# Kernel tuning notes

Hardware: AMD Instinct MI355X
Metric: run time of the kernel (lower is better)

Reference implementation:

```python
import jax, jax.numpy as jnp
import numpy as np

NUM_HEADS = 12
DIM = 768
HEAD_DIM = DIM // NUM_HEADS
SCALE = HEAD_DIM ** -0.5
LORA_ALPHA = 1.0


def setup_inputs() -> dict:
    key = jax.random.key(0)
    ks = jax.random.split(key, 9)
    B, H, W = 1, 64, 64
    return {
        "x": jax.random.normal(ks[0], (B, H, W, DIM), jnp.float32),
        "w_qkv": jax.random.normal(ks[1], (3 * DIM, DIM), jnp.float32) * 0.02,
        "b_qkv": jax.random.normal(ks[2], (3 * DIM,), jnp.float32) * 0.02,
        "lora_A": jax.random.normal(ks[3], (12, DIM), jnp.float32) * 0.02,
        "lora_B": jax.random.normal(ks[4], (3 * DIM, 12), jnp.float32) * 0.02,
        "w_proj": jax.random.normal(ks[5], (DIM, DIM), jnp.float32) * 0.02,
        "b_proj": jax.random.normal(ks[6], (DIM,), jnp.float32) * 0.02,
        "rel_pos_h": jax.random.normal(ks[7], (2 * H - 1, HEAD_DIM), jnp.float32) * 0.02,
        "rel_pos_w": jax.random.normal(ks[8], (2 * W - 1, HEAD_DIM), jnp.float32) * 0.02,
    }


def _get_rel_pos(size: int, rel_pos: jnp.ndarray) -> jnp.ndarray:
    # q_size == k_size and rel_pos.shape[0] == 2*size-1, so no interpolation.
    coords = jnp.arange(size)[:, None] - jnp.arange(size)[None, :] + (size - 1)
    return rel_pos[coords]  # [size, size, head_dim]


def reference(x, w_qkv, b_qkv, lora_A, lora_B, w_proj, b_proj, rel_pos_h, rel_pos_w):
    B, H, W, _ = x.shape
    N = H * W
    # LoRA qkv projection: W_eff path = base + alpha * x @ (B A)^T
    qkv = x @ w_qkv.T + b_qkv + LORA_ALPHA * ((x @ lora_A.T) @ lora_B.T)
    qkv = qkv.reshape(B, N, 3, NUM_HEADS, HEAD_DIM)
    qkv = jnp.transpose(qkv, (2, 0, 3, 1, 4)).reshape(3, B * NUM_HEADS, N, HEAD_DIM)
    q, k, v = qkv[0], qkv[1], qkv[2]
    attn = jnp.einsum('bqc,bkc->bqk', q * SCALE, k)  # [B*nh, N, N]
    # decomposed relative position bias
    Rh = _get_rel_pos(H, rel_pos_h)  # [H, H, hd]
    Rw = _get_rel_pos(W, rel_pos_w)  # [W, W, hd]
    r_q = q.reshape(B * NUM_HEADS, H, W, HEAD_DIM)
    rel_h = jnp.einsum('bhwc,hkc->bhwk', r_q, Rh)
    rel_w = jnp.einsum('bhwc,wkc->bhwk', r_q, Rw)
    attn = (attn.reshape(-1, H, W, H, W)
            + rel_h[:, :, :, :, None]
            + rel_w[:, :, :, None, :]).reshape(-1, N, N)
    attn = jax.nn.softmax(attn, axis=-1)
    out = jnp.einsum('bqk,bkc->bqc', attn, v)  # [B*nh, N, hd]
    out = out.reshape(B, NUM_HEADS, H, W, HEAD_DIM)
    out = jnp.transpose(out, (0, 2, 3, 1, 4)).reshape(B, H, W, DIM)
    return out @ w_proj.T + b_proj
```

## Files before the change

### kernel.cpp

```cpp
#include <hip/hip_runtime.h>
#include <stdint.h>


typedef __attribute__((ext_vector_type(4))) float f32x4;
typedef __attribute__((ext_vector_type(16))) float f32x16;
typedef __attribute__((ext_vector_type(4))) float fvec4;
typedef __attribute__((ext_vector_type(8))) short s16x8;
typedef __attribute__((ext_vector_type(4))) short s16x4;
typedef __attribute__((ext_vector_type(4))) unsigned u32x4;

constexpr int NH  = 12;
constexpr int HD  = 64;
constexpr int DIM = 768;
constexpr int N   = 4096;
constexpr int QKV = 2304;
constexpr float LOG2E  = 1.4426950408889634f;
constexpr float SCALE2 = 0.125f * LOG2E;

static __device__ __forceinline__ short f2bf(float f) {
  unsigned u = __builtin_bit_cast(unsigned, f);
  unsigned r = (u + 0x7FFFu + ((u >> 16) & 1u)) >> 16;
  return (short)r;
}
static __device__ __forceinline__ float bf2f(short s) {
  unsigned u = ((unsigned)(unsigned short)s) << 16;
  return __builtin_bit_cast(float, u);
}
static __device__ __forceinline__ unsigned cvt_pk_bf16(float a, float b) {
  unsigned r;
  asm("v_cvt_pk_bf16_f32 %0, %1, %2" : "=v"(r) : "v"(a), "v"(b));
  return r;
}
static __device__ __forceinline__ float ex2(float x) {
  float r;
  asm("v_exp_f32 %0, %1" : "=v"(r) : "v"(x));
  return r;
}
static __device__ __forceinline__ void gload16(const void* g, void* l) {
  __builtin_amdgcn_global_load_lds(
      (const __attribute__((address_space(1))) void*)g,
      (__attribute__((address_space(3))) void*)l, 16, 0, 0);
}
static __device__ __forceinline__ void barrier_pre() {
  __builtin_amdgcn_s_barrier();
  __builtin_amdgcn_sched_barrier(0);
}
static __device__ __forceinline__ void barrier_post() {
  __builtin_amdgcn_sched_barrier(0);
  __builtin_amdgcn_s_barrier();
  __builtin_amdgcn_sched_barrier(0);
}

__global__ __launch_bounds__(256) void k_weff(const float* __restrict__ w_qkv,
                                              const float* __restrict__ lora_A,
                                              const float* __restrict__ lora_B,
                                              short* __restrict__ weff) {
  int e = blockIdx.x * 256 + threadIdx.x;
  if (e >= QKV * DIM) return;
  int r = e / DIM, c = e % DIM;
  float acc = w_qkv[e];
#pragma unroll
  for (int t = 0; t < 12; ++t) acc += lora_B[r * 12 + t] * lora_A[t * DIM + c];
  weff[e] = f2bf(acc);
}

__global__ __launch_bounds__(256) void k_x2bf(const float* __restrict__ x,
                                              short* __restrict__ xb) {
  int i = blockIdx.x * 256 + threadIdx.x;
  fvec4 v = *reinterpret_cast<const fvec4*>(x + (size_t)i * 4);
  s16x4 p;
  p[0] = f2bf(v[0]); p[1] = f2bf(v[1]); p[2] = f2bf(v[2]); p[3] = f2bf(v[3]);
  *reinterpret_cast<s16x4*>(xb + (size_t)i * 4) = p;
}

__global__ __launch_bounds__(256) void k_wsplit(const float* __restrict__ w,
                                                short* __restrict__ ws) {
  int r = blockIdx.y;
  int kk = blockIdx.x * 256 + threadIdx.x;
  int blk = (kk >= 1536) ? 2 : (kk >= 768 ? 1 : 0);
  int c = kk - blk * 768;
  float wv = w[(size_t)r * 768 + c];
  short hi = f2bf(wv);
  ws[(size_t)r * 2304 + kk] = (blk == 1) ? f2bf(wv - bf2f(hi)) : hi;
}

template <int KIT, int MODE, int BM>
__global__ __launch_bounds__(256, 2) void k_gemm(const short* __restrict__ A,
                                                 const short* __restrict__ B,
                                                 const float* __restrict__ bias,
                                                 short* __restrict__ qo,
                                                 short* __restrict__ ko,
                                                 short* __restrict__ vo,
                                                 float* __restrict__ outf) {
  constexpr int MFR = BM / 32;
  constexpr int BUFB = BM * 128 + 16384;
  __shared__ __align__(16) char lds[2 * BUFB];
  const int tid = threadIdx.x;
  const int wave = tid >> 6, lane = tid & 63, lr = lane & 15, lg = lane >> 4;
  const int wr = wave >> 1, wc = wave & 1;
  const int i0 = blockIdx.x * BM, j0 = blockIdx.y * 128;
  const int LDA = KIT * 128;

  size_t offA[MFR], offB[4];
#pragma unroll
  for (int it = 0; it < MFR; ++it) {
    int c = it * 256 + tid;
    int row = c >> 3;
    offA[it] = (size_t)row * LDA + (((c & 7) << 4) ^ ((row & 7) << 4));
  }
#pragma unroll
  for (int it = 0; it < 4; ++it) {
    int c = it * 256 + tid;
    int row = c >> 3;
    offB[it] = (size_t)row * LDA + (((c & 7) << 4) ^ ((row & 7) << 4));
  }
  const char* Ab = (const char*)A + (size_t)i0 * LDA;
  const char* Bb = (const char*)B + (size_t)j0 * LDA;

  auto STAGE = [&](int kt, int b) {
    char* base = lds + b * BUFB;
    const size_t kadd = (size_t)kt * 128;
#pragma unroll
    for (int it = 0; it < MFR; ++it)
      gload16(Ab + kadd + offA[it], base + wave * 1024 + it * 4096);
#pragma unroll
    for (int it = 0; it < 4; ++it)
      gload16(Bb + kadd + offB[it], base + BM * 128 + wave * 1024 + it * 4096);
  };

  const int swz = (lr & 7) << 4;
  const int ab = (wr * (BM / 2) + lr) * 128 + ((lg * 16) ^ swz);
  const int bb = BM * 128 + (wc * 64 + lr) * 128 + ((lg * 16) ^ swz);

  f32x4 acc[MFR][4] = {};

  STAGE(0, 0);
  for (int kt = 0; kt < KIT; ++kt) {
    const int buf = kt & 1;
    if (kt + 1 < KIT) {
      STAGE(kt + 1, buf ^ 1);
      if constexpr (BM == 128)
        asm volatile("s_waitcnt vmcnt(8)" ::: "memory");
      else
        asm volatile("s_waitcnt vmcnt(6)" ::: "memory");
    } else {
      asm volatile("s_waitcnt vmcnt(0)" ::: "memory");
    }
    barrier_pre();
    const char* bufp = lds + buf * BUFB;
#pragma unroll
    for (int ks2 = 0; ks2 < 2; ++ks2) {
      s16x8 af[MFR], bf_[4];
#pragma unroll
      for (int m = 0; m < MFR; ++m)
        af[m] = *reinterpret_cast<const s16x8*>(bufp + ((ab + m * 2048) ^ (ks2 << 6)));
#pragma unroll
      for (int n = 0; n < 4; ++n)
        bf_[n] = *reinterpret_cast<const s16x8*>(bufp + ((bb + n * 2048) ^ (ks2 << 6)));
#pragma unroll
      for (int m = 0; m < MFR; ++m)
#pragma unroll
        for (int n = 0; n < 4; ++n)
          acc[m][n] = __builtin_amdgcn_mfma_f32_16x16x32_bf16(af[m], bf_[n], acc[m][n], 0, 0, 0);
    }
    barrier_post();
  }

  if constexpr (MODE == 0) {
    const int three = j0 / 768;
    const int head = ((j0 % 768) >> 6) + wc;
    const float osc = (three == 1) ? SCALE2 : 1.0f;
    short* dst = (three == 0) ? qo : ((three == 1) ? ko : vo);
#pragma unroll
    for (int n = 0; n < 4; ++n) {
      const int col = n * 16 + lr;
      const float bj = bias[j0 + wc * 64 + col];
#pragma unroll
      for (int m = 0; m < MFR; ++m)
#pragma unroll
        for (int r = 0; r < 4; ++r) {
          int i = i0 + wr * (BM / 2) + m * 16 + lg * 4 + r;
          dst[((size_t)head * N + i) * HD + col] = f2bf((acc[m][n][r] + bj) * osc);
        }
    }
  } else {
#pragma unroll
    for (int n = 0; n < 4; ++n) {
      const int j = j0 + wc * 64 + n * 16 + lr;
      const float bj = bias[j];
#pragma unroll
      for (int m = 0; m < MFR; ++m)
#pragma unroll
        for (int r = 0; r < 4; ++r) {
          int i = i0 + wr * (BM / 2) + m * 16 + lg * 4 + r;
          outf[(size_t)i * 768 + j] = acc[m][n][r] + bj;
        }
    }
  }
}

__global__ __launch_bounds__(256) void k_vT(const short* __restrict__ vg,
                                            short* __restrict__ vTg) {
  __shared__ short ts[64 * 72];
  const int tid = threadIdx.x;
  const int i0 = blockIdx.x * 64;
  const int h = blockIdx.y;
#pragma unroll
  for (int it = 0; it < 2; ++it) {
    int ch = tid + 256 * it;
    int row = ch >> 3, cc = (ch & 7) * 8;
    *reinterpret_cast<s16x8*>(&ts[row * 72 + cc]) =
        *reinterpret_cast<const s16x8*>(&vg[((size_t)h * N + i0 + row) * HD + cc]);
  }
  __syncthreads();
#pragma unroll
  for (int it = 0; it < 2; ++it) {
    int ch = tid + 256 * it;
    int c = ch >> 3, ii = (ch & 7) * 8;
    s16x8 o;
#pragma unroll
    for (int j = 0; j < 8; ++j) o[j] = ts[(ii + j) * 72 + c];
    *reinterpret_cast<s16x8*>(&vTg[((size_t)h * HD + c) * N + i0 + ii]) = o;
  }
}

__global__ __launch_bounds__(256) void k_relh(const short* __restrict__ qg,
                                              const float* __restrict__ tab,
                                              short* __restrict__ rhT) {
  __shared__ short Ts[64 * 72];
  const int tid = threadIdx.x;
  const int wave = tid >> 6, lane = tid & 63, lr = lane & 15, lg = lane >> 4;
  const int h = blockIdx.x >> 6, qh = blockIdx.x & 63;
#pragma unroll
  for (int it = 0; it < 4; ++it) {
    int e = tid + 256 * it;
    int row = e >> 4, c4 = (e & 15) * 4;
    fvec4 v = *reinterpret_cast<const fvec4*>(tab + (size_t)(qh + 63 - row) * 64 + c4);
    s16x4 p;
    p[0] = f2bf(v[0]); p[1] = f2bf(v[1]); p[2] = f2bf(v[2]); p[3] = f2bf(v[3]);
    *reinterpret_cast<s16x4*>(&Ts[row * 72 + c4]) = p;
  }
  __syncthreads();
  const size_t qrow = (size_t)h * N + qh * 64 + wave * 16 + lr;
  const s16x8 a0 = *reinterpret_cast<const s16x8*>(qg + qrow * 64 + lg * 8);
  const s16x8 a1 = *reinterpret_cast<const s16x8*>(qg + qrow * 64 + 32 + lg * 8);
  f32x4 acc[4] = {};
#pragma unroll
  for (int ks2 = 0; ks2 < 2; ++ks2)
#pragma unroll
    for (int n = 0; n < 4; ++n) {
      s16x8 b = *reinterpret_cast<const s16x8*>(&Ts[(n * 16 + lr) * 72 + ks2 * 32 + lg * 8]);
      acc[n] = __builtin_amdgcn_mfma_f32_16x16x32_bf16(ks2 ? a1 : a0, b, acc[n], 0, 0, 0);
    }
  const size_t ob = ((size_t)(h * 64 + qh)) * 4096;
#pragma unroll
  for (int n = 0; n < 4; ++n) {
    s16x4 o;
#pragma unroll
    for (int r = 0; r < 4; ++r) o[r] = f2bf(acc[n][r] * LOG2E);
    *reinterpret_cast<s16x4*>(&rhT[ob + (size_t)(n * 16 + lr) * 64 + wave * 16 + lg * 4]) = o;
  }
}

__global__ __launch_bounds__(256) void k_relw(const short* __restrict__ qg,
                                              const float* __restrict__ tab,
                                              short* __restrict__ rwg) {
  __shared__ short Ts[128 * 72];
  const int tid = threadIdx.x;
  const int wave = tid >> 6, lane = tid & 63, lr = lane & 15, lg = lane >> 4;
  const int h = blockIdx.x >> 6, qh = blockIdx.x & 63;
#pragma unroll
  for (int it = 0; it < 8; ++it) {
    int e = tid + 256 * it;
    int row = e >> 4, c4 = (e & 15) * 4;
    s16x4 p = {0, 0, 0, 0};
    if (row < 127) {
      fvec4 v = *reinterpret_cast<const fvec4*>(tab + (size_t)row * 64 + c4);
      p[0] = f2bf(v[0]); p[1] = f2bf(v[1]); p[2] = f2bf(v[2]); p[3] = f2bf(v[3]);
    }
    *reinterpret_cast<s16x4*>(&Ts[row * 72 + c4]) = p;
  }
  __syncthreads();
  const size_t qrow = (size_t)h * N + qh * 64 + wave * 16 + lr;
  const s16x8 a0 = *reinterpret_cast<const s16x8*>(qg + qrow * 64 + lg * 8);
  const s16x8 a1 = *reinterpret_cast<const s16x8*>(qg + qrow * 64 + 32 + lg * 8);
  f32x4 acc[8] = {};
#pragma unroll
  for (int ks2 = 0; ks2 < 2; ++ks2)
#pragma unroll
    for (int n = 0; n < 8; ++n) {
      s16x8 b = *reinterpret_cast<const s16x8*>(&Ts[(n * 16 + lr) * 72 + ks2 * 32 + lg * 8]);
      acc[n] = __builtin_amdgcn_mfma_f32_16x16x32_bf16(ks2 ? a1 : a0, b, acc[n], 0, 0, 0);
    }
  const size_t ob = ((size_t)h * N + qh * 64) * 64;
#pragma unroll
  for (int n = 0; n < 8; ++n) {
    int d = n * 16 + lr;
#pragma unroll
    for (int r = 0; r < 4; ++r) {
      int qw = wave * 16 + lg * 4 + r;
      int kw = qw + 63 - d;
      if ((unsigned)kw < 64u) rwg[ob + (size_t)qw * 64 + kw] = f2bf(acc[n][r] * LOG2E);
    }
  }
}

#define QG_BLOCK(QB0, QB1, QB2, QB3, RW, RH2, ACC0, ACC1, LA, LB)              \
  do {                                                                         \
    f32x16 sa = {};                                                            \
    __builtin_amdgcn_s_setprio(1);                                             \
    sa = __builtin_amdgcn_mfma_f32_32x32x16_bf16(kf0, QB0, sa, 0, 0, 0);       \
    sa = __builtin_amdgcn_mfma_f32_32x32x16_bf16(kf1, QB1, sa, 0, 0, 0);       \
    sa = __builtin_amdgcn_mfma_f32_32x32x16_bf16(kf2, QB2, sa, 0, 0, 0);       \
    sa = __builtin_amdgcn_mfma_f32_32x32x16_bf16(kf3, QB3, sa, 0, 0, 0);       \
    __builtin_amdgcn_s_setprio(0);                                             \
    float p[16];                                                               \
    _Pragma("unroll")                                                          \
    for (int reg = 0; reg < 16; ++reg)                                         \
      p[reg] = ex2(sa[reg] + RH2 + RW[reg]);                                   \
    float t0 = (p[0] + p[1]) + (p[2] + p[3]);                                  \
    float t1 = (p[4] + p[5]) + (p[6] + p[7]);                                  \
    float t2 = (p[8] + p[9]) + (p[10] + p[11]);                                \
    float t3 = (p[12] + p[13]) + (p[14] + p[15]);                              \
    LA += t0 + t1;                                                             \
    LB += t2 + t3;                                                             \
    unsigned w00 = cvt_pk_bf16(p[0], p[1]),   w01 = cvt_pk_bf16(p[2], p[3]);   \
    unsigned w10 = cvt_pk_bf16(p[4], p[5]),   w11 = cvt_pk_bf16(p[6], p[7]);   \
    unsigned w20 = cvt_pk_bf16(p[8], p[9]),   w21 = cvt_pk_bf16(p[10], p[11]); \
    unsigned w30 = cvt_pk_bf16(p[12], p[13]), w31 = cvt_pk_bf16(p[14], p[15]); \
    asm("v_permlane32_swap_b32 %0, %1" : "+v"(w00), "+v"(w10));                \
    asm("v_permlane32_swap_b32 %0, %1" : "+v"(w01), "+v"(w11));                \
    asm("v_permlane32_swap_b32 %0, %1" : "+v"(w20), "+v"(w30));                \
    asm("v_permlane32_swap_b32 %0, %1" : "+v"(w21), "+v"(w31));                \
    u32x4 u0 = {w00, w01, w10, w11};                                           \
    u32x4 u1 = {w20, w21, w30, w31};                                           \
    s16x8 pa0 = __builtin_bit_cast(s16x8, u0);                                 \
    s16x8 pa1 = __builtin_bit_cast(s16x8, u1);                                 \
    __builtin_amdgcn_s_setprio(1);                                             \
    ACC0 = __builtin_amdgcn_mfma_f32_32x32x16_bf16(pa0, vf0, ACC0, 0, 0, 0);   \
    ACC0 = __builtin_amdgcn_mfma_f32_32x32x16_bf16(pa1, vf2, ACC0, 0, 0, 0);   \
    ACC1 = __builtin_amdgcn_mfma_f32_32x32x16_bf16(pa0, vf1, ACC1, 0, 0, 0);   \
    ACC1 = __builtin_amdgcn_mfma_f32_32x32x16_bf16(pa1, vf3, ACC1, 0, 0, 0);   \
    __builtin_amdgcn_s_setprio(0);                                             \
  } while (0)

__global__ __launch_bounds__(256, 2) void k_flash(const short* __restrict__ qg,
                                                  const short* __restrict__ kg,
                                                  const short* __restrict__ vTg,
                                                  const short* __restrict__ rhTg,
                                                  const short* __restrict__ rwg,
                                                  short* __restrict__ aprime) {
  __shared__ __align__(16) char lds[65536];
  const int tid = threadIdx.x;
  const int wave = tid >> 6, lane = tid & 63;
  const int ql = lane & 31, hi = lane >> 5;
  const int kt2 = wave & 1, kh2 = wave >> 1;
  const int bid = blockIdx.x;
  const int id = (bid & 7) * 96 + (bid >> 3);
  const int h = id >> 6, qt = id & 63;
  const int i0 = qt * 64;

  const short* q0p = qg + ((size_t)h * N + i0 + ql) * 64 + hi * 8;
  const short* q1p = q0p + 32 * 64;
  const s16x8 qb00 = *reinterpret_cast<const s16x8*>(q0p);
  const s16x8 qb01 = *reinterpret_cast<const s16x8*>(q0p + 16);
  const s16x8 qb02 = *reinterpret_cast<const s16x8*>(q0p + 32);
  const s16x8 qb03 = *reinterpret_cast<const s16x8*>(q0p + 48);
  const s16x8 qb10 = *reinterpret_cast<const s16x8*>(q1p);
  const s16x8 qb11 = *reinterpret_cast<const s16x8*>(q1p + 16);
  const s16x8 qb12 = *reinterpret_cast<const s16x8*>(q1p + 32);
  const s16x8 qb13 = *reinterpret_cast<const s16x8*>(q1p + 48);

  f32x16 rw0, rw1;
  {
    const short* rwp0 = rwg + ((size_t)h * N + i0 + ql) * 64 + kh2 * 32 + hi * 4;
    const short* rwp1 = rwp0 + 32 * 64;
#pragma unroll
    for (int reg = 0; reg < 16; ++reg) {
      int o = (reg & 3) + 8 * (reg >> 2);
      rw0[reg] = bf2f(rwp0[o]);
      rw1[reg] = bf2f(rwp1[o]);
    }
  }
  const short* rhp = rhTg + ((size_t)(h * 64 + qt)) * 4096;

  int soff[8];
  const char* sbase;
  if (wave < 2) {
    sbase = (const char*)kg + (size_t)h * N * 128 + wave * 64 * 128;
#pragma unroll
    for (int it = 0; it < 8; ++it) {
      int c = it * 64 + lane, row = c >> 3;
      soff[it] = row * 128 + (((c & 7) << 4) ^ ((row & 7) << 4));
    }
  } else {
    sbase = (const char*)vTg + (size_t)h * 64 * 8192 + (wave - 2) * 128;
#pragma unroll
    for (int it = 0; it < 8; ++it) {
      int c = it * 64 + lane, r = c >> 3;
      soff[it] = r * 8192 + (((c & 7) << 4) ^ ((r & 7) << 4));
    }
  }
  const int sstep = (wave < 2) ? 16384 : 256;
  char* lreg = lds + wave * 8192;

  auto STAGE = [&](int i, int buf) {
    const char* sp = sbase + (size_t)i * sstep;
    char* lp = lreg + buf * 32768;
#pragma unroll
    for (int it = 0; it < 8; ++it) gload16(sp + soff[it], lp + it * 1024);
  };

  const int swzq = (ql & 7) << 4;
  const int krow = (kt2 * 64 + kh2 * 32 + ql) * 128;
  const int kco0 = krow + ((0 * 32 + hi * 16) ^ swzq);
  const int kco1 = krow + ((1 * 32 + hi * 16) ^ swzq);
  const int kco2 = krow + ((2 * 32 + hi * 16) ^ swzq);
  const int kco3 = krow + ((3 * 32 + hi * 16) ^ swzq);
  const int vrow0 = 16384 + kt2 * 8192 + ql * 128;
  const int vrow1 = vrow0 + 32 * 128;
  const int vch0 = (kh2 * 64 + 0 * 32 + hi * 16) ^ swzq;
  const int vch1 = (kh2 * 64 + 1 * 32 + hi * 16) ^ swzq;
  const int vco0 = vrow0 + vch0;
  const int vco1 = vrow1 + vch0;
  const int vco2 = vrow0 + vch1;
  const int vco3 = vrow1 + vch1;

  f32x16 acc00 = {}, acc01 = {}, acc10 = {}, acc11 = {};
  float la0 = 0.f, lb0 = 0.f, la1 = 0.f, lb1 = 0.f;

  unsigned short rhc0 = (unsigned short)rhp[(size_t)kt2 * 64 + ql];
  unsigned short rhc1 = (unsigned short)rhp[(size_t)kt2 * 64 + 32 + ql];

  STAGE(0, 0);
  __syncthreads();

  for (int i = 0; i < 32; ++i) {
    const int buf = i & 1;
    if (i + 1 < 32) STAGE(i + 1, buf ^ 1);
    const int nx = (i + 1 < 32) ? i + 1 : 31;
    unsigned short rhn0 = (unsigned short)rhp[(size_t)(nx * 2 + kt2) * 64 + ql];
    unsigned short rhn1 = (unsigned short)rhp[(size_t)(nx * 2 + kt2) * 64 + 32 + ql];

    const char* bufp = lds + buf * 32768;
    s16x8 kf0 = *reinterpret_cast<const s16x8*>(bufp + kco0);
    s16x8 kf1 = *reinterpret_cast<const s16x8*>(bufp + kco1);
    s16x8 kf2 = *reinterpret_cast<const s16x8*>(bufp + kco2);
    s16x8 kf3 = *reinterpret_cast<const s16x8*>(bufp + kco3);
    s16x8 vf0 = *reinterpret_cast<const s16x8*>(bufp + vco0);
    s16x8 vf1 = *reinterpret_cast<const s16x8*>(bufp + vco1);
    s16x8 vf2 = *reinterpret_cast<const s16x8*>(bufp + vco2);
    s16x8 vf3 = *reinterpret_cast<const s16x8*>(bufp + vco3);

    const float rh20 = bf2f((short)rhc0);
    const float rh21 = bf2f((short)rhc1);

    QG_BLOCK(qb00, qb01, qb02, qb03, rw0, rh20, acc00, acc01, la0, lb0);
    QG_BLOCK(qb10, qb11, qb12, qb13, rw1, rh21, acc10, acc11, la1, lb1);

    rhc0 = rhn0; rhc1 = rhn1;
    __syncthreads();
  }

  float l0 = la0 + lb0, l1 = la1 + lb1;
  l0 += __shfl_xor(l0, 32);
  l1 += __shfl_xor(l1, 32);
  float* LS = (float*)lds;
  if (lane < 32) {
    LS[wave * 64 + ql] = l0;
    LS[wave * 64 + 32 + ql] = l1;
  }
  __syncthreads();
  const int eq = wave * 16 + (lane >> 2);
  const int cb = (lane & 3) * 16;
  float inv = 1.0f / (LS[eq] + LS[64 + eq] + LS[128 + eq] + LS[192 + eq]);
  __syncthreads();
  float* OF = (float*)lds;
#pragma unroll
  for (int qg2 = 0; qg2 < 2; ++qg2)
#pragma unroll
    for (int ct = 0; ct < 2; ++ct) {
      const f32x16& a = qg2 ? (ct ? acc11 : acc10) : (ct ? acc01 : acc00);
#pragma unroll
      for (int reg = 0; reg < 16; ++reg) {
        int q = qg2 * 32 + (reg & 3) + 8 * (reg >> 2) + 4 * hi;
        int c = ct * 32 + ql;
        OF[wave * 4096 + q * 64 + (c ^ ((q & 7) << 2))] = a[reg];
      }
    }
  __syncthreads();
  f32x4 osum[4] = {};
#pragma unroll
  for (int w = 0; w < 4; ++w)
#pragma unroll
    for (int j = 0; j < 4; ++j)
      osum[j] += *reinterpret_cast<const f32x4*>(
          &OF[w * 4096 + eq * 64 + ((cb + j * 4) ^ ((eq & 7) << 2))]);

  s16x8 hi8[2], lo8[2];
#pragma unroll
  for (int j = 0; j < 4; ++j)
#pragma unroll
    for (int e = 0; e < 4; ++e) {
      float o = osum[j][e] * inv;
      short oh = f2bf(o);
      float lo = o - bf2f(oh);
      int idx = j * 4 + e;
      hi8[idx >> 3][idx & 7] = oh;
      lo8[idx >> 3][idx & 7] = f2bf(lo);
    }
  size_t obase = (size_t)(i0 + eq) * 2304 + h * 64 + cb;
  *reinterpret_cast<s16x8*>(&aprime[obase]) = hi8[0];
  *reinterpret_cast<s16x8*>(&aprime[obase + 8]) = hi8[1];
  *reinterpret_cast<s16x8*>(&aprime[obase + 768]) = hi8[0];
  *reinterpret_cast<s16x8*>(&aprime[obase + 776]) = hi8[1];
  *reinterpret_cast<s16x8*>(&aprime[obase + 1536]) = lo8[0];
  *reinterpret_cast<s16x8*>(&aprime[obase + 1544]) = lo8[1];
}

extern "C" void kernel_launch(void* const* d_in, const int* in_sizes, int n_in,
                              void* d_out, int out_size, void* d_ws, size_t ws_size,
                              hipStream_t stream) {
  const float* x      = (const float*)d_in[0];
  const float* w_qkv  = (const float*)d_in[1];
  const float* b_qkv  = (const float*)d_in[2];
  const float* lora_A = (const float*)d_in[3];
  const float* lora_B = (const float*)d_in[4];
  const float* w_proj = (const float*)d_in[5];
  const float* b_proj = (const float*)d_in[6];
  const float* rel_h  = (const float*)d_in[7];
  const float* rel_w  = (const float*)d_in[8];
  float* out = (float*)d_out;

  char* ws = (char*)d_ws;
  short* weff   = (short*)(ws + 0);
  short* xb     = (short*)(ws + 3538944);
  short* vg     = (short*)(ws + 9830400);
  short* aprime = (short*)(ws + 0);
  short* qg     = (short*)(ws + 18874368);
  short* kg     = (short*)(ws + 25165824);
  short* vTg    = (short*)(ws + 31457280);
  short* rhT    = (short*)(ws + 37748736);
  short* rwg    = (short*)(ws + 44040192);
  short* wsp    = (short*)(ws + 50331648);
  (void)ws_size; (void)in_sizes; (void)n_in; (void)out_size;

  k_weff<<<dim3((QKV * DIM + 255) / 256), dim3(256), 0, stream>>>(w_qkv, lora_A, lora_B, weff);
  k_x2bf<<<dim3(3072), dim3(256), 0, stream>>>(x, xb);
  k_wsplit<<<dim3(9, 768), dim3(256), 0, stream>>>(w_proj, wsp);
  k_gemm<12, 0, 128><<<dim3(32, 18), dim3(256), 0, stream>>>(xb, weff, b_qkv, qg, kg, vg, nullptr);
  k_vT<<<dim3(64, NH), dim3(256), 0, stream>>>(vg, vTg);
  k_relh<<<dim3(NH * 64), dim3(256), 0, stream>>>(qg, rel_h, rhT);
  k_relw<<<dim3(NH * 64), dim3(256), 0, stream>>>(qg, rel_w, rwg);
  k_flash<<<dim3(NH * 64), dim3(256), 0, stream>>>(qg, kg, vTg, rhT, rwg, aprime);
  k_gemm<36, 1, 64><<<dim3(64, 6), dim3(256), 0, stream>>>(aprime, wsp, b_proj, nullptr, nullptr, nullptr, out);
}
```

Baseline: 161.0 us.

## Single-buffer V tiles and split epilogue reduction to shrink LDS to 48KB

Keeps K double-buffered but gives V a single buffer that is refilled after each iteration's compute, behind an extra barrier. The epilogue's cross-wave reduction now handles the two column halves in turn through a smaller LDS scratch area. Total shared memory drops from 64KB to 48KB, which is meant to let more blocks fit per CU. The cost is that the V load is no longer overlapped with compute, and each iteration now has an extra synchronization.

```diff
diff --git a/kernel.cpp b/kernel.cpp
--- a/kernel.cpp
+++ b/kernel.cpp
@@ -350,7 +350,7 @@
                                                   const short* __restrict__ rhTg,
                                                   const short* __restrict__ rwg,
                                                   short* __restrict__ aprime) {
-  __shared__ __align__(16) char lds[65536];
+  __shared__ __align__(16) char lds[49152];
   const int tid = threadIdx.x;
   const int wave = tid >> 6, lane = tid & 63;
   const int ql = lane & 31, hi = lane >> 5;
@@ -401,14 +401,22 @@
       soff[it] = r * 8192 + (((c & 7) << 4) ^ ((r & 7) << 4));
     }
   }
-  const int sstep = (wave < 2) ? 16384 : 256;
-  char* lreg = lds + wave * 8192;
-
-  auto STAGE = [&](int i, int buf) {
-    const char* sp = sbase + (size_t)i * sstep;
-    char* lp = lreg + buf * 32768;
-#pragma unroll
-    for (int it = 0; it < 8; ++it) gload16(sp + soff[it], lp + it * 1024);
+
+  auto STAGE_K = [&](int i, int buf) {
+    if (wave < 2) {
+      const char* sp = sbase + (size_t)i * 16384;
+      char* lp = lds + wave * 8192 + buf * 16384;
+#pragma unroll
+      for (int it = 0; it < 8; ++it) gload16(sp + soff[it], lp + it * 1024);
+    }
+  };
+  auto STAGE_V = [&](int i) {
+    if (wave >= 2) {
+      const char* sp = sbase + (size_t)i * 256;
+      char* lp = lds + 32768 + (wave - 2) * 8192;
+#pragma unroll
+      for (int it = 0; it < 8; ++it) gload16(sp + soff[it], lp + it * 1024);
+    }
   };
 
   const int swzq = (ql & 7) << 4;
@@ -417,14 +425,13 @@
   const int kco1 = krow + ((1 * 32 + hi * 16) ^ swzq);
   const int kco2 = krow + ((2 * 32 + hi * 16) ^ swzq);
   const int kco3 = krow + ((3 * 32 + hi * 16) ^ swzq);
-  const int vrow0 = 16384 + kt2 * 8192 + ql * 128;
-  const int vrow1 = vrow0 + 32 * 128;
+  const int vbase = 32768 + kt2 * 8192 + ql * 128;
   const int vch0 = (kh2 * 64 + 0 * 32 + hi * 16) ^ swzq;
   const int vch1 = (kh2 * 64 + 1 * 32 + hi * 16) ^ swzq;
-  const int vco0 = vrow0 + vch0;
-  const int vco1 = vrow1 + vch0;
-  const int vco2 = vrow0 + vch1;
-  const int vco3 = vrow1 + vch1;
+  const int vco0 = vbase + vch0;
+  const int vco1 = vbase + 4096 + vch0;
+  const int vco2 = vbase + vch1;
+  const int vco3 = vbase + 4096 + vch1;
 
   f32x16 acc00 = {}, acc01 = {}, acc10 = {}, acc11 = {};
   float la0 = 0.f, lb0 = 0.f, la1 = 0.f, lb1 = 0.f;
@@ -432,25 +439,26 @@
   unsigned short rhc0 = (unsigned short)rhp[(size_t)kt2 * 64 + ql];
   unsigned short rhc1 = (unsigned short)rhp[(size_t)kt2 * 64 + 32 + ql];
 
-  STAGE(0, 0);
+  STAGE_K(0, 0);
+  STAGE_V(0);
   __syncthreads();
 
   for (int i = 0; i < 32; ++i) {
     const int buf = i & 1;
-    if (i + 1 < 32) STAGE(i + 1, buf ^ 1);
+    if (i + 1 < 32) STAGE_K(i + 1, buf ^ 1);
     const int nx = (i + 1 < 32) ? i + 1 : 31;
     unsigned short rhn0 = (unsigned short)rhp[(size_t)(nx * 2 + kt2) * 64 + ql];
     unsigned short rhn1 = (unsigned short)rhp[(size_t)(nx * 2 + kt2) * 64 + 32 + ql];
 
-    const char* bufp = lds + buf * 32768;
+    const char* bufp = lds + buf * 16384;
     s16x8 kf0 = *reinterpret_cast<const s16x8*>(bufp + kco0);
     s16x8 kf1 = *reinterpret_cast<const s16x8*>(bufp + kco1);
     s16x8 kf2 = *reinterpret_cast<const s16x8*>(bufp + kco2);
     s16x8 kf3 = *reinterpret_cast<const s16x8*>(bufp + kco3);
-    s16x8 vf0 = *reinterpret_cast<const s16x8*>(bufp + vco0);
-    s16x8 vf1 = *reinterpret_cast<const s16x8*>(bufp + vco1);
-    s16x8 vf2 = *reinterpret_cast<const s16x8*>(bufp + vco2);
-    s16x8 vf3 = *reinterpret_cast<const s16x8*>(bufp + vco3);
+    s16x8 vf0 = *reinterpret_cast<const s16x8*>(lds + vco0);
+    s16x8 vf1 = *reinterpret_cast<const s16x8*>(lds + vco1);
+    s16x8 vf2 = *reinterpret_cast<const s16x8*>(lds + vco2);
+    s16x8 vf3 = *reinterpret_cast<const s16x8*>(lds + vco3);
 
     const float rh20 = bf2f((short)rhc0);
     const float rh21 = bf2f((short)rhc1);
@@ -460,8 +468,13 @@
 
     rhc0 = rhn0; rhc1 = rhn1;
     __syncthreads();
-  }
-
+    if (i + 1 < 32) {
+      STAGE_V(i + 1);
+      __syncthreads();
+    }
+  }
+
+  __syncthreads();
   float l0 = la0 + lb0, l1 = la1 + lb1;
   l0 += __shfl_xor(l0, 32);
   l1 += __shfl_xor(l1, 32);
@@ -471,51 +484,45 @@
     LS[wave * 64 + 32 + ql] = l1;
   }
   __syncthreads();
-  const int eq = wave * 16 + (lane >> 2);
-  const int cb = (lane & 3) * 16;
+  const int eq = tid >> 2;
+  const int cq = (tid & 3) * 8;
   float inv = 1.0f / (LS[eq] + LS[64 + eq] + LS[128 + eq] + LS[192 + eq]);
-  __syncthreads();
-  float* OF = (float*)lds;
-#pragma unroll
-  for (int qg2 = 0; qg2 < 2; ++qg2)
-#pragma unroll
-    for (int ct = 0; ct < 2; ++ct) {
-      const f32x16& a = qg2 ? (ct ? acc11 : acc10) : (ct ? acc01 : acc00);
-#pragma unroll
-      for (int reg = 0; reg < 16; ++reg) {
-        int q = qg2 * 32 + (reg & 3) + 8 * (reg >> 2) + 4 * hi;
-        int c = ct * 32 + ql;
-        OF[wave * 4096 + q * 64 + (c ^ ((q & 7) << 2))] = a[reg];
-      }
-    }
-  __syncthreads();
-  f32x4 osum[4] = {};
-#pragma unroll
-  for (int w = 0; w < 4; ++w)
-#pragma unroll
-    for (int j = 0; j < 4; ++j)
-      osum[j] += *reinterpret_cast<const f32x4*>(
-          &OF[w * 4096 + eq * 64 + ((cb + j * 4) ^ ((eq & 7) << 2))]);
-
-  s16x8 hi8[2], lo8[2];
-#pragma unroll
-  for (int j = 0; j < 4; ++j)
-#pragma unroll
-    for (int e = 0; e < 4; ++e) {
-      float o = osum[j][e] * inv;
+  float* OF = (float*)(lds + 4096);
+  const size_t obase = (size_t)(i0 + eq) * 2304 + h * 64;
+
+#pragma unroll
+  for (int ct = 0; ct < 2; ++ct) {
+    __syncthreads();
+    const f32x16& a0 = ct ? acc01 : acc00;
+    const f32x16& a1 = ct ? acc11 : acc10;
+#pragma unroll
+    for (int reg = 0; reg < 16; ++reg) {
+      int qr = (reg & 3) + 8 * (reg >> 2) + 4 * hi;
+      int sw = (qr & 3) << 3;
+      OF[wave * 2048 + qr * 32 + (ql ^ sw)] = a0[reg];
+      OF[wave * 2048 + (32 + qr) * 32 + (ql ^ sw)] = a1[reg];
+    }
+    __syncthreads();
+    float osum[8];
+#pragma unroll
+    for (int j = 0; j < 8; ++j) {
+      int cs = (cq + j) ^ ((eq & 3) << 3);
+      osum[j] = OF[eq * 32 + cs] + OF[2048 + eq * 32 + cs] +
+                OF[4096 + eq * 32 + cs] + OF[6144 + eq * 32 + cs];
+    }
+    s16x8 h8, l8;
+#pragma unroll
+    for (int j = 0; j < 8; ++j) {
+      float o = osum[j] * inv;
       short oh = f2bf(o);
-      float lo = o - bf2f(oh);
-      int idx = j * 4 + e;
-      hi8[idx >> 3][idx & 7] = oh;
-      lo8[idx >> 3][idx & 7] = f2bf(lo);
-    }
-  size_t obase = (size_t)(i0 + eq) * 2304 + h * 64 + cb;
-  *reinterpret_cast<s16x8*>(&aprime[obase]) = hi8[0];
-  *reinterpret_cast<s16x8*>(&aprime[obase + 8]) = hi8[1];
-  *reinterpret_cast<s16x8*>(&aprime[obase + 768]) = hi8[0];
-  *reinterpret_cast<s16x8*>(&aprime[obase + 776]) = hi8[1];
-  *reinterpret_cast<s16x8*>(&aprime[obase + 1536]) = lo8[0];
-  *reinterpret_cast<s16x8*>(&aprime[obase + 1544]) = lo8[1];
+      h8[j] = oh;
+      l8[j] = f2bf(o - bf2f(oh));
+    }
+    size_t ob2 = obase + ct * 32 + cq;
+    *reinterpret_cast<s16x8*>(&aprime[ob2]) = h8;
+    *reinterpret_cast<s16x8*>(&aprime[ob2 + 768]) = h8;
+    *reinterpret_cast<s16x8*>(&aprime[ob2 + 1536]) = l8;
+  }
 }
 
 extern "C" void kernel_launch(void* const* d_in, const int* in_sizes, int n_in,
```

New measurement: 171.9 us. 1.07x slower.
